# Performance work log

Measured on AMD Instinct MI355X. Metric: run time of the kernel, lower is better.

Reference implementation:

```python
import jax, jax.numpy as jnp
import numpy as np

EPS = 1e-5
NEG_SLOPE = 0.2

def _linear(x, w, b):
    return x @ w.T + b

def _seg_softmax(a, dst, n):
    # numerically stable softmax over edges grouped by destination node
    m = jax.ops.segment_max(a, dst, num_segments=n)
    e = jnp.exp(a - m[dst])
    s = jax.ops.segment_sum(e, dst, num_segments=n)
    return e / (s[dst] + 1e-16)

def _gat(x, src, dst, n, w, a_src, a_dst, b):
    # PyG GATConv, heads=1: h = xW^T; alpha = LeakyReLU(a_s.h_src + a_d.h_dst)
    h = x @ w.T                                   # [N,H]
    al_s = (h * a_src).sum(-1)                    # [N]
    al_d = (h * a_dst).sum(-1)                    # [N]
    alpha = jax.nn.leaky_relu(al_s[src] + al_d[dst], NEG_SLOPE)  # [E]
    attn = _seg_softmax(alpha, dst, n)
    out = jax.ops.segment_sum(attn[:, None] * h[src], dst, num_segments=n)
    return out + b

def _bn(x, g, b):
    # BatchNorm over the node dimension (training-style batch stats, eval dropout)
    mu = x.mean(0)
    var = x.var(0)
    return (x - mu) * jax.lax.rsqrt(var + EPS) * g + b

def setup_inputs() -> dict:
    key = jax.random.key(0)
    N, E, SAT, NEI, H, OUT = 50000, 1600000, 32, 32, 128, 16
    ks = jax.random.split(key, 26)
    p = lambda k, shape, s=0.05: jax.random.normal(k, shape, jnp.float32) * s
    return {
        "x": jax.random.normal(ks[0], (N, SAT + NEI), jnp.float32),
        "edge_index": jax.random.randint(ks[1], (2, E), 0, N, jnp.int32),
        "sat_w": p(ks[2], (H, SAT)), "sat_b": jnp.zeros((H,), jnp.float32),
        "neigh_w": p(ks[3], (H, NEI)), "neigh_b": jnp.zeros((H,), jnp.float32),
        "fus_w": p(ks[4], (1, 2 * H)), "fus_b": jnp.zeros((1,), jnp.float32),
        "w1": p(ks[5], (H, H)), "as1": p(ks[6], (H,)), "ad1": p(ks[7], (H,)), "b1": jnp.zeros((H,), jnp.float32),
        "g1": jnp.ones((H,), jnp.float32), "be1": jnp.zeros((H,), jnp.float32),
        "w2": p(ks[8], (H, H)), "as2": p(ks[9], (H,)), "ad2": p(ks[10], (H,)), "b2": jnp.zeros((H,), jnp.float32),
        "g2": jnp.ones((H,), jnp.float32), "be2": jnp.zeros((H,), jnp.float32),
        "fc1_w": p(ks[11], (H, H)), "fc1_b": jnp.zeros((H,), jnp.float32),
        "fc2_w": p(ks[12], (OUT, H)), "fc2_b": jnp.zeros((OUT,), jnp.float32),
    }

def reference(x, edge_index, sat_w, sat_b, neigh_w, neigh_b, fus_w, fus_b,
              w1, as1, ad1, b1, g1, be1, w2, as2, ad2, b2, g2, be2,
              fc1_w, fc1_b, fc2_w, fc2_b):
    n = x.shape[0]
    sat_dim = sat_w.shape[1]
    sat = jax.nn.relu(_linear(x[:, :sat_dim], sat_w, sat_b))
    nei = jax.nn.relu(_linear(x[:, sat_dim:], neigh_w, neigh_b))
    gate = jax.nn.sigmoid(_linear(jnp.concatenate([sat, nei], axis=1), fus_w, fus_b))
    h = gate * sat + (1.0 - gate) * nei
    # GATConv adds self-loops by default
    loops = jnp.arange(n, dtype=edge_index.dtype)
    src = jnp.concatenate([edge_index[0], loops])
    dst = jnp.concatenate([edge_index[1], loops])
    res = h
    h = jax.nn.relu(_bn(_gat(h, src, dst, n, w1, as1, ad1, b1), g1, be1)) + res
    res = h
    h = jax.nn.relu(_bn(_gat(h, src, dst, n, w2, as2, ad2, b2), g2, be2)) + res
    h = jax.nn.relu(_linear(h, fc1_w, fc1_b))
    return _linear(h, fc2_w, fc2_b)
```

## Files before the change

kernel.cpp:

```cpp
#include <hip/hip_runtime.h>

#define H 128

typedef __attribute__((ext_vector_type(8))) short bf16x8;
typedef __attribute__((ext_vector_type(4))) float f32x4;

__device__ __forceinline__ float bf2f(unsigned short u) {
    return __uint_as_float(((unsigned)u) << 16);
}
__device__ __forceinline__ unsigned short f2bf(float f) {
    unsigned u = __float_as_uint(f);
    unsigned r = (u + 0x7fffu + ((u >> 16) & 1u)) >> 16;
    return (unsigned short)r;
}
__device__ __forceinline__ unsigned pack2bf(float a, float b) {
    return (unsigned)f2bf(a) | ((unsigned)f2bf(b) << 16);
}

__global__ void fill_u32(unsigned* __restrict__ p, unsigned v, int n) {
    int i = blockIdx.x * blockDim.x + threadIdx.x;
    if (i < n) p[i] = v;
}

__global__ void fuse_kernel(const float* __restrict__ x,
                            const float* __restrict__ sat_w, const float* __restrict__ sat_b,
                            const float* __restrict__ neigh_w, const float* __restrict__ neigh_b,
                            const float* __restrict__ fus_w, const float* __restrict__ fus_b,
                            unsigned short* __restrict__ h0b, int N) {
    __shared__ unsigned smem[8512];
    __shared__ float reds[4][64];
    unsigned* a_lds = smem;
    unsigned* w_lds = smem + 2304;
    int tid = threadIdx.x;
    int base = blockIdx.x * 64;
    for (int i = tid; i < 64 * 32; i += 256) {
        int n = i >> 5, kp = i & 31;
        int gn = base + n;
        float2 v = (gn < N) ? *(const float2*)(x + (size_t)gn * 64 + kp * 2) : make_float2(0.f, 0.f);
        a_lds[n * 36 + kp] = pack2bf(v.x, v.y);
    }
    for (int i = tid; i < 256 * 16; i += 256) {
        int r = i >> 4, kp = i & 15;
        const float* wsrc = (r < 128) ? (sat_w + (size_t)r * 32) : (neigh_w + (size_t)(r - 128) * 32);
        float2 v = *(const float2*)(wsrc + kp * 2);
        w_lds[r * 20 + kp] = pack2bf(v.x, v.y);
    }
    __syncthreads();
    int lane = tid & 63;
    int wv = tid >> 6;
    int lr = lane & 15, lk = lane >> 4;
    f32x4 accS[4][2], accN[4][2];
#pragma unroll
    for (int r = 0; r < 4; ++r)
#pragma unroll
        for (int t = 0; t < 2; ++t) {
            accS[r][t] = (f32x4){0.f, 0.f, 0.f, 0.f};
            accN[r][t] = (f32x4){0.f, 0.f, 0.f, 0.f};
        }
    bf16x8 afS[4], afN[4];
#pragma unroll
    for (int r = 0; r < 4; ++r) {
        afS[r] = *(const bf16x8*)&a_lds[(r * 16 + lr) * 36 + lk * 4];
        afN[r] = *(const bf16x8*)&a_lds[(r * 16 + lr) * 36 + 16 + lk * 4];
    }
#pragma unroll
    for (int t = 0; t < 2; ++t) {
        bf16x8 bS = *(const bf16x8*)&w_lds[(wv * 32 + t * 16 + lr) * 20 + lk * 4];
        bf16x8 bN = *(const bf16x8*)&w_lds[(128 + wv * 32 + t * 16 + lr) * 20 + lk * 4];
#pragma unroll
        for (int r = 0; r < 4; ++r) {
            accS[r][t] = __builtin_amdgcn_mfma_f32_16x16x32_bf16(afS[r], bS, accS[r][t], 0, 0, 0);
            accN[r][t] = __builtin_amdgcn_mfma_f32_16x16x32_bf16(afN[r], bN, accN[r][t], 0, 0, 0);
        }
    }
    __syncthreads();
    unsigned short* cst = (unsigned short*)smem;
#pragma unroll
    for (int t = 0; t < 2; ++t) {
        int col = wv * 32 + t * 16 + lr;
        float sb = sat_b[col], nb = neigh_b[col];
#pragma unroll
        for (int r = 0; r < 4; ++r) {
#pragma unroll
            for (int j = 0; j < 4; ++j) {
                int srow = r * 16 + lk * 4 + j;
                cst[srow * 266 + col] = f2bf(fmaxf(accS[r][t][j] + sb, 0.f));
                cst[srow * 266 + 133 + col] = f2bf(fmaxf(accN[r][t][j] + nb, 0.f));
            }
        }
    }
    __syncthreads();
    int node = tid & 63;
    int part = tid >> 6;
    float ps = 0.f;
#pragma unroll
    for (int k = 0; k < 32; ++k) {
        int col = part * 32 + k;
        ps += bf2f(cst[node * 266 + col]) * fus_w[col]
            + bf2f(cst[node * 266 + 133 + col]) * fus_w[128 + col];
    }
    reds[part][node] = ps;
    __syncthreads();
    float tot = reds[0][node] + reds[1][node] + reds[2][node] + reds[3][node];
    float g = 1.f / (1.f + __expf(-(tot + fus_b[0])));
    if (base + node < N) {
        unsigned* op = (unsigned*)h0b + (size_t)(base + node) * 64 + part * 16;
#pragma unroll
        for (int kp = 0; kp < 16; ++kp) {
            int col = part * 32 + kp * 2;
            float o0 = g * bf2f(cst[node * 266 + col]) + (1.f - g) * bf2f(cst[node * 266 + 133 + col]);
            float o1 = g * bf2f(cst[node * 266 + col + 1]) + (1.f - g) * bf2f(cst[node * 266 + 134 + col]);
            op[kp] = pack2bf(o0, o1);
        }
    }
}

template <int TAG, int MODE>
__global__ void gemm128m(const void* __restrict__ inv, const float* __restrict__ w,
                         const float* __restrict__ bias, int do_relu,
                         unsigned short* __restrict__ outb, int N,
                         const float* __restrict__ a_sp, const float* __restrict__ a_dp,
                         float* __restrict__ al_s, float* __restrict__ al_d,
                         const float* __restrict__ bns, const unsigned short* __restrict__ resb,
                         unsigned* __restrict__ yout) {
    __shared__ unsigned a_lds[64 * 68];
    __shared__ unsigned w_lds[128 * 68];
    __shared__ float reds[4][64];
    __shared__ float redd[4][64];
    int tid = threadIdx.x;
    int base = blockIdx.x * 64;
    for (int i = tid; i < 64 * 64; i += 256) {
        int n = i >> 6, kp = i & 63;
        int gn = base + n;
        unsigned p = 0u;
        if (gn < N) {
            if (MODE == 1) {
                p = ((const unsigned*)inv)[(size_t)gn * 64 + kp];
            } else {
                float2 v = *(const float2*)((const float*)inv + (size_t)gn * 128 + kp * 2);
                float2 sc = ((const float2*)bns)[kp];
                float2 sh = ((const float2*)(bns + 128))[kp];
                ushort2 rr = ((const ushort2*)(resb + (size_t)gn * 128))[kp];
                float y0 = fmaxf(v.x * sc.x + sh.x, 0.f) + bf2f(rr.x);
                float y1 = fmaxf(v.y * sc.y + sh.y, 0.f) + bf2f(rr.y);
                p = pack2bf(y0, y1);
                if (yout) yout[(size_t)gn * 64 + kp] = p;
            }
        }
        a_lds[n * 68 + kp] = p;
    }
    for (int i = tid; i < 128 * 64; i += 256) {
        int c = i >> 6, kp = i & 63;
        float2 v = *(const float2*)(w + (size_t)c * 128 + kp * 2);
        w_lds[c * 68 + kp] = pack2bf(v.x, v.y);
    }
    __syncthreads();
    int lane = tid & 63;
    int wv = tid >> 6;
    int lr = lane & 15;
    int lk = lane >> 4;
    f32x4 acc[4][2];
#pragma unroll
    for (int r = 0; r < 4; ++r)
#pragma unroll
        for (int t = 0; t < 2; ++t) acc[r][t] = (f32x4){0.f, 0.f, 0.f, 0.f};
    for (int c = 0; c < 4; ++c) {
        bf16x8 af[4], bfr[2];
#pragma unroll
        for (int r = 0; r < 4; ++r)
            af[r] = *(const bf16x8*)&a_lds[(r * 16 + lr) * 68 + c * 16 + lk * 4];
#pragma unroll
        for (int t = 0; t < 2; ++t)
            bfr[t] = *(const bf16x8*)&w_lds[(wv * 32 + t * 16 + lr) * 68 + c * 16 + lk * 4];
#pragma unroll
        for (int r = 0; r < 4; ++r)
#pragma unroll
            for (int t = 0; t < 2; ++t)
                acc[r][t] = __builtin_amdgcn_mfma_f32_16x16x32_bf16(af[r], bfr[t], acc[r][t], 0, 0, 0);
    }
    __syncthreads();
    unsigned short* cst = (unsigned short*)a_lds;
#pragma unroll
    for (int t = 0; t < 2; ++t) {
        int col = wv * 32 + t * 16 + lr;
        float bv = bias ? bias[col] : 0.f;
#pragma unroll
        for (int r = 0; r < 4; ++r) {
#pragma unroll
            for (int j = 0; j < 4; ++j) {
                float v = acc[r][t][j] + bv;
                if (do_relu) v = fmaxf(v, 0.f);
                cst[(r * 16 + lk * 4 + j) * 136 + col] = f2bf(v);
            }
        }
    }
    __syncthreads();
    for (int i = tid; i < 64 * 64; i += 256) {
        int n = i >> 6, kp = i & 63;
        int gn = base + n;
        if (gn < N) ((unsigned*)outb)[(size_t)gn * 64 + kp] = a_lds[n * 68 + kp];
    }
    if (a_sp) {
        int node = tid & 63;
        int part = tid >> 6;
        float ps = 0.f, pd = 0.f;
        int kb = part * 32;
        const unsigned short* xr = cst + node * 136 + kb;
#pragma unroll
        for (int k = 0; k < 32; ++k) {
            float v = bf2f(xr[k]);
            ps += v * a_sp[kb + k];
            pd += v * a_dp[kb + k];
        }
        reds[part][node] = ps;
        redd[part][node] = pd;
        __syncthreads();
        if (tid < 64) {
            int gn = base + tid;
            if (gn < N) {
                al_s[gn] = reds[0][tid] + reds[1][tid] + reds[2][tid] + reds[3][tid];
                al_d[gn] = redd[0][tid] + redd[1][tid] + redd[2][tid] + redd[3][tid];
            }
        }
    }
}

#define SCB 256
#define NBUK 196
#define BCAP 10240
__global__ void pack_hist_bucket(const int* __restrict__ src, const int* __restrict__ dst,
                                 unsigned* __restrict__ pkb, int* __restrict__ cnt8,
                                 int* __restrict__ bukCur, int E, int N, int CH) {
    __shared__ int lcnt[NBUK];
    __shared__ int lbase[NBUK];
    int tid = threadIdx.x;
    int blk = blockIdx.x;
    int e0 = blk * CH;
    int e1 = min(e0 + CH, E);
    int hcopy = blk & 7;
    for (int sb = e0; sb < e1; sb += 4096) {
        int nsc = min(4096, e1 - sb);
        unsigned pkv[16];
        int rk[16], bb[16];
        for (int i = tid; i < NBUK; i += 256) lcnt[i] = 0;
        __syncthreads();
#pragma unroll
        for (int i = 0; i < 16; ++i) {
            int off = tid + i * 256;
            bb[i] = -1;
            if (off < nsc) {
                int e = sb + off;
                int s = src[e];
                int d = dst[e];
                atomicAdd(cnt8 + (size_t)hcopy * N + d, 1);
                pkv[i] = ((unsigned)d << 16) | (unsigned)s;
                int b = d >> 8;
                bb[i] = b;
                rk[i] = atomicAdd(&lcnt[b], 1);
            }
        }
        __syncthreads();
        for (int i = tid; i < NBUK; i += 256) lbase[i] = atomicAdd(&bukCur[i], lcnt[i]);
        __syncthreads();
#pragma unroll
        for (int i = 0; i < 16; ++i) {
            if (bb[i] >= 0) {
                pkb[(size_t)bb[i] * BCAP + lbase[bb[i]] + rk[i]] = pkv[i];
            }
        }
        __syncthreads();
    }
}

__global__ void scan_a(const int* __restrict__ cnt8, int* __restrict__ nodeoff,
                       int* __restrict__ blocksum, int N) {
    int i = blockIdx.x * SCB + threadIdx.x;
    int tot = 0;
    if (i < N) {
#pragma unroll
        for (int c = 0; c < 8; ++c) tot += cnt8[(size_t)c * N + i];
    }
    __shared__ int tmp[SCB];
    tmp[threadIdx.x] = tot;
    __syncthreads();
    for (int off = 1; off < SCB; off <<= 1) {
        int t = (threadIdx.x >= off) ? tmp[threadIdx.x - off] : 0;
        __syncthreads();
        tmp[threadIdx.x] += t;
        __syncthreads();
    }
    if (i < N) nodeoff[i] = tmp[threadIdx.x] - tot;
    if (threadIdx.x == SCB - 1) blocksum[blockIdx.x] = tmp[SCB - 1];
}

__global__ void scan_b(const int* __restrict__ blocksum, int* __restrict__ blockoff,
                       int* __restrict__ rowptrN, int NB) {
    __shared__ int tmp[1024];
    int t = threadIdx.x;
    int v = (t < NB) ? blocksum[t] : 0;
    tmp[t] = v;
    __syncthreads();
    for (int off = 1; off < 1024; off <<= 1) {
        int u = (t >= off) ? tmp[t - off] : 0;
        __syncthreads();
        tmp[t] += u;
        __syncthreads();
    }
    if (t < NB) blockoff[t] = tmp[t] - v;
    if (t == 1023) *rowptrN = tmp[1023];
}

__global__ void scan_c(const int* __restrict__ nodeoff, const int* __restrict__ blockoff,
                       int* __restrict__ rowptr, float* __restrict__ accum2, int N) {
    if (blockIdx.x < 16) {
        accum2[blockIdx.x * 256 + threadIdx.x] = 0.f;
    }
    int i = blockIdx.x * SCB + threadIdx.x;
    if (i >= N) return;
    rowptr[i] = blockoff[blockIdx.x] + nodeoff[i];
}

__global__ void scatter_sort(const unsigned* __restrict__ pkb, const int* __restrict__ bukCnt,
                             const int* __restrict__ rowptr, int* __restrict__ ssrc, int N) {
    __shared__ int lcur[256];
    __shared__ int tmp[256];
    __shared__ int osrc[BCAP];
    int b = blockIdx.x;
    int d0 = b << 8;
    int cnt = bukCnt[b];
    const unsigned* base = pkb + (size_t)b * BCAP;
    int tid = threadIdx.x;
    lcur[tid] = 0;
    __syncthreads();
    for (int i = tid; i < cnt; i += 256)
        atomicAdd(&lcur[(int)(base[i] >> 16) - d0], 1);
    __syncthreads();
    int v = lcur[tid];
    tmp[tid] = v;
    __syncthreads();
    for (int off = 1; off < 256; off <<= 1) {
        int u = (tid >= off) ? tmp[tid - off] : 0;
        __syncthreads();
        tmp[tid] += u;
        __syncthreads();
    }
    lcur[tid] = tmp[tid] - v;
    __syncthreads();
    for (int i = tid; i < cnt; i += 256) {
        unsigned p = base[i];
        int ld = (int)(p >> 16) - d0;
        int pos = atomicAdd(&lcur[ld], 1);
        osrc[pos] = (int)(p & 0xFFFFu);
    }
    __syncthreads();
    int gbase = rowptr[d0];
    for (int i = tid; i < cnt; i += 256)
        ssrc[gbase + i] = osrc[i];
}

template <int TAG>
__global__ void gat_agg(const int* __restrict__ rowptr, const int* __restrict__ ssrc,
                        const float* __restrict__ al_s, const float* __restrict__ al_d,
                        const unsigned short* __restrict__ hb, float* __restrict__ out,
                        float* __restrict__ accum8, int N) {
    __shared__ int s_sv[4][64];
    __shared__ float s_ev[4][64];
    __shared__ float ys[4][128];
    __shared__ float yq[4][128];
    int tid = threadIdx.x;
    int wiw = tid >> 6;
    int w = (blockIdx.x * blockDim.x + tid) >> 6;
    int lane = tid & 63;
    int sub = lane >> 5;
    int fl = lane & 31;
    float a0 = 0.f, a1 = 0.f, a2 = 0.f, a3 = 0.f;
    float ss = 0.f;
    if (w < N) {
        int beg = rowptr[w], end = rowptr[w + 1];
        float ald = al_d[w];
        float a_self = al_s[w] + ald;
        a_self = (a_self > 0.f) ? a_self : 0.2f * a_self;
        float m = a_self;
        for (int e = beg + lane; e < end; e += 64) {
            float a = al_s[ssrc[e]] + ald;
            a = (a > 0.f) ? a : 0.2f * a;
            m = fmaxf(m, a);
        }
        for (int off = 32; off; off >>= 1) m = fmaxf(m, __shfl_xor(m, off));
        for (int base = beg; base < end; base += 64) {
            int nch = min(64, end - base);
            int sv = 0;
            float ev = 0.f;
            if (lane < nch) {
                sv = ssrc[base + lane];
                float a = al_s[sv] + ald;
                a = (a > 0.f) ? a : 0.2f * a;
                ev = __expf(a - m);
            }
            ss += ev;
            s_sv[wiw][lane] = sv;
            s_ev[wiw][lane] = ev;
            for (int j0 = 0; j0 < nch; j0 += 8) {
                ushort4 hv[4];
                float evv[4];
#pragma unroll
                for (int jj = 0; jj < 4; ++jj) {
                    int j = j0 + 2 * jj + sub;
                    bool ok = j < nch;
                    int svj = ok ? s_sv[wiw][j] : 0;
                    evv[jj] = ok ? s_ev[wiw][j] : 0.f;
                    hv[jj] = ((const ushort4*)(hb + (size_t)svj * H))[fl];
                }
#pragma unroll
                for (int jj = 0; jj < 4; ++jj) {
                    a0 += evv[jj] * bf2f(hv[jj].x);
                    a1 += evv[jj] * bf2f(hv[jj].y);
                    a2 += evv[jj] * bf2f(hv[jj].z);
                    a3 += evv[jj] * bf2f(hv[jj].w);
                }
            }
        }
        for (int off = 32; off; off >>= 1) ss += __shfl_xor(ss, off);
        a0 += __shfl_xor(a0, 32);
        a1 += __shfl_xor(a1, 32);
        a2 += __shfl_xor(a2, 32);
        a3 += __shfl_xor(a3, 32);
        float ev_self = __expf(a_self - m);
        ss += ev_self;
        ushort4 hs = ((const ushort4*)(hb + (size_t)w * H))[fl];
        a0 += ev_self * bf2f(hs.x);
        a1 += ev_self * bf2f(hs.y);
        a2 += ev_self * bf2f(hs.z);
        a3 += ev_self * bf2f(hs.w);
        float inv = 1.f / (ss + 1e-16f);
        a0 *= inv; a1 *= inv; a2 *= inv; a3 *= inv;
        if (sub == 0) {
            ((float4*)(out + (size_t)w * H))[fl] = make_float4(a0, a1, a2, a3);
        }
    }
    if (sub == 0) {
        float4 yy = (w < N) ? make_float4(a0, a1, a2, a3) : make_float4(0.f, 0.f, 0.f, 0.f);
        ((float4*)&ys[wiw][0])[fl] = yy;
        ((float4*)&yq[wiw][0])[fl] = make_float4(yy.x * yy.x, yy.y * yy.y, yy.z * yy.z, yy.w * yy.w);
    }
    __syncthreads();
    if (tid < 128) {
        float s = ys[0][tid] + ys[1][tid] + ys[2][tid] + ys[3][tid];
        float q = yq[0][tid] + yq[1][tid] + yq[2][tid] + yq[3][tid];
        float* ac = accum8 + (size_t)(blockIdx.x & 7) * 256;
        atomicAdd(ac + tid, s);
        atomicAdd(ac + 128 + tid, q);
    }
}

__global__ void bn_finalize(const float* __restrict__ accum8, const float* __restrict__ g,
                            const float* __restrict__ be, float* __restrict__ bns, int N) {
    int tid = threadIdx.x;
    if (tid >= 128) return;
    float s = 0.f, q = 0.f;
#pragma unroll
    for (int c = 0; c < 8; ++c) {
        s += accum8[c * 256 + tid];
        q += accum8[c * 256 + 128 + tid];
    }
    float Ninv = 1.f / (float)N;
    float mu = s * Ninv;
    float var = q * Ninv - mu * mu;
    float rsig = rsqrtf(var + 1e-5f);
    float sc = rsig * g[tid];
    bns[tid] = sc;
    bns[128 + tid] = be[tid] - mu * sc;
}

__global__ void fc2_kernel(const unsigned short* __restrict__ in, const float* __restrict__ w,
                           const float* __restrict__ b, float* __restrict__ out,
                           int N, int OUT) {
    __shared__ float wsm[16 * 132];
    __shared__ float xs[16][129];
    int tid = threadIdx.x;
    for (int i = tid; i < OUT * H; i += 256) {
        int o = i >> 7, k = i & 127;
        wsm[o * 132 + k] = w[i];
    }
    int nb = blockIdx.x * 16;
    for (int i = tid; i < 16 * 128; i += 256) {
        int n = i >> 7, k = i & 127;
        int gn = nb + n;
        xs[n][k] = (gn < N) ? bf2f(in[(size_t)gn * H + k]) : 0.f;
    }
    __syncthreads();
    int o = tid & 15;
    int nn = tid >> 4;
    int n = nb + nn;
    if (n >= N || o >= OUT) return;
    const float* xr = xs[nn];
    const float* wr = wsm + o * 132;
    float acc = b[o];
#pragma unroll 8
    for (int k = 0; k < H; k += 4) {
        acc += xr[k] * wr[k] + xr[k + 1] * wr[k + 1] + xr[k + 2] * wr[k + 2] + xr[k + 3] * wr[k + 3];
    }
    out[(size_t)n * OUT + o] = acc;
}


extern "C" void kernel_launch(void* const* d_in, const int* in_sizes, int n_in,
                              void* d_out, int out_size, void* d_ws, size_t ws_size,
                              hipStream_t stream) {
    const float* x       = (const float*)d_in[0];
    const int*   ei      = (const int*)d_in[1];
    const float* sat_w   = (const float*)d_in[2];
    const float* sat_b   = (const float*)d_in[3];
    const float* neigh_w = (const float*)d_in[4];
    const float* neigh_b = (const float*)d_in[5];
    const float* fus_w   = (const float*)d_in[6];
    const float* fus_b   = (const float*)d_in[7];
    const float* w1      = (const float*)d_in[8];
    const float* as1     = (const float*)d_in[9];
    const float* ad1     = (const float*)d_in[10];
    const float* g1      = (const float*)d_in[12];
    const float* be1     = (const float*)d_in[13];
    const float* w2      = (const float*)d_in[14];
    const float* as2     = (const float*)d_in[15];
    const float* ad2     = (const float*)d_in[16];
    const float* g2      = (const float*)d_in[18];
    const float* be2     = (const float*)d_in[19];
    const float* fc1_w   = (const float*)d_in[20];
    const float* fc1_b   = (const float*)d_in[21];
    const float* fc2_w   = (const float*)d_in[22];
    const float* fc2_b   = (const float*)d_in[23];

    int N = in_sizes[0] / 64;
    int E = in_sizes[1] / 2;
    int OUT = in_sizes[23];
    int NB = (N + SCB - 1) / SCB;
    int CH = (E + 255) / 256;
    int NBUKET = (N + 255) >> 8;

    float* ws    = (float*)d_ws;
    float* h0    = ws;
    float* hA    = h0 + (size_t)N * H;
    float* agg   = hA + (size_t)N * H;
    float* al_s  = agg + (size_t)N * H;
    float* al_d  = al_s + N;
    float* accum = al_d + N;
    float* bns1  = accum + 4096;
    float* bns2  = bns1 + 256;
    int* rowptr  = (int*)(bns2 + 256);
    int* cnt8    = rowptr + (N + 1);
    int* bukCur  = cnt8 + (size_t)8 * N;
    int* nodeoff = bukCur + NBUK;
    int* blocksum= nodeoff + N;
    int* blockoff= blocksum + NB;
    int* ssrc    = blockoff + NB;
    unsigned* pkb= (unsigned*)(ssrc + E);
    unsigned* y1b= pkb + (size_t)NBUK * BCAP;
    unsigned short* hAb = (unsigned short*)hA;
    unsigned short* h0b = (unsigned short*)(hA + (size_t)N * 64);

    const int* srcp = ei;
    const int* dstp = ei + E;

    dim3 b256(256);
    int gGemm = (N + 63) / 64;
    int gWaveN = (N + 3) / 4;

    fuse_kernel<<<gGemm, b256, 0, stream>>>(x, sat_w, sat_b, neigh_w, neigh_b, fus_w, fus_b, h0b, N);

    fill_u32<<<(8 * N + NBUK + 255) / 256, b256, 0, stream>>>((unsigned*)cnt8, 0u, 8 * N + NBUK);
    pack_hist_bucket<<<256, b256, 0, stream>>>(srcp, dstp, pkb, cnt8, bukCur, E, N, CH);
    scan_a<<<NB, SCB, 0, stream>>>(cnt8, nodeoff, blocksum, N);
    scan_b<<<1, 1024, 0, stream>>>(blocksum, blockoff, rowptr + N, NB);
    scan_c<<<NB, SCB, 0, stream>>>(nodeoff, blockoff, rowptr, accum, N);
    scatter_sort<<<NBUKET, b256, 0, stream>>>(pkb, bukCur, rowptr, ssrc, N);

    gemm128m<1, 1><<<gGemm, b256, 0, stream>>>(h0b, w1, nullptr, 0, hAb, N, as1, ad1, al_s, al_d,
                                               nullptr, nullptr, nullptr);
    gat_agg<1><<<gWaveN, b256, 0, stream>>>(rowptr, ssrc, al_s, al_d, hAb, agg, accum, N);
    bn_finalize<<<1, 128, 0, stream>>>(accum, g1, be1, bns1, N);

    gemm128m<2, 2><<<gGemm, b256, 0, stream>>>(agg, w2, nullptr, 0, hAb, N, as2, ad2, al_s, al_d,
                                               bns1, h0b, y1b);
    gat_agg<2><<<gWaveN, b256, 0, stream>>>(rowptr, ssrc, al_s, al_d, hAb, h0, accum + 2048, N);
    bn_finalize<<<1, 128, 0, stream>>>(accum + 2048, g2, be2, bns2, N);

    gemm128m<3, 2><<<gGemm, b256, 0, stream>>>(h0, fc1_w, fc1_b, 1, hAb, N, nullptr, nullptr,
                                               nullptr, nullptr, bns2, (const unsigned short*)y1b,
                                               nullptr);
    fc2_kernel<<<(N + 15) / 16, b256, 0, stream>>>(hAb, fc2_w, fc2_b, (float*)d_out, N, OUT);
}
```

Before: 351.9 us.

## Replace global-atomic CSR build with two-pass local bucket sort

Rebuilds the destination-sorted edge list (CSR) used by the GAT aggregation. Each block now partitions its chunk of edges into 256 buckets in shared memory and records per-block bucket counts and offsets. A single-block kernel then scans the bucket totals, and each bucket block gathers its segments by binary search and computes rowptr locally. This drops the per-node global atomic histogram, the zero-fill and the three-kernel scan, cutting kernel launches and global atomic traffic. In exchange, the bucket-base scan runs serially in one block, and every gathered element pays for a binary search.

```diff
diff --git a/kernel.cpp b/kernel.cpp
--- a/kernel.cpp
+++ b/kernel.cpp
@@ -15,11 +15,6 @@
 }
 __device__ __forceinline__ unsigned pack2bf(float a, float b) {
     return (unsigned)f2bf(a) | ((unsigned)f2bf(b) << 16);
-}
-
-__global__ void fill_u32(unsigned* __restrict__ p, unsigned v, int n) {
-    int i = blockIdx.x * blockDim.x + threadIdx.x;
-    if (i < n) p[i] = v;
 }
 
 __global__ void fuse_kernel(const float* __restrict__ x,
@@ -225,115 +220,107 @@
     }
 }
 
-#define SCB 256
-#define NBUK 196
+#define PBMAX 6400
+#define NBSTR 256
+__global__ void pack_bucket(const int* __restrict__ src, const int* __restrict__ dst,
+                            unsigned* __restrict__ pk2, int* __restrict__ cntBB,
+                            int* __restrict__ offBB, int E, int PB) {
+    __shared__ unsigned opk[PBMAX];
+    __shared__ unsigned opk2[PBMAX];
+    __shared__ int lcnt[256];
+    __shared__ int tmp[256];
+    int tid = threadIdx.x;
+    int blk = blockIdx.x;
+    int e0 = blk * PB;
+    int n = min(PB, E - e0);
+    if (n < 0) n = 0;
+    lcnt[tid] = 0;
+    __syncthreads();
+    for (int i = tid; i < n; i += 256) {
+        int s = src[e0 + i];
+        int d = dst[e0 + i];
+        unsigned p = ((unsigned)d << 16) | (unsigned)s;
+        opk[i] = p;
+        atomicAdd(&lcnt[d >> 8], 1);
+    }
+    __syncthreads();
+    int v = lcnt[tid];
+    tmp[tid] = v;
+    __syncthreads();
+    for (int off = 1; off < 256; off <<= 1) {
+        int u = (tid >= off) ? tmp[tid - off] : 0;
+        __syncthreads();
+        tmp[tid] += u;
+        __syncthreads();
+    }
+    int excl = tmp[tid] - v;
+    cntBB[(size_t)blk * NBSTR + tid] = v;
+    offBB[(size_t)blk * NBSTR + tid] = excl;
+    lcnt[tid] = excl;
+    __syncthreads();
+    for (int i = tid; i < n; i += 256) {
+        unsigned p = opk[i];
+        int pos = atomicAdd(&lcnt[(p >> 16) >> 8], 1);
+        opk2[pos] = p;
+    }
+    __syncthreads();
+    for (int i = tid; i < n; i += 256) pk2[e0 + i] = opk2[i];
+}
+
+__global__ void bucket_base(const int* __restrict__ cntBB, int* __restrict__ bbase,
+                            int* __restrict__ rowptr, float* __restrict__ accum,
+                            int E, int N, int NBLK) {
+    __shared__ int tmp[256];
+    int tid = threadIdx.x;
+    for (int i = tid; i < 4096; i += 256) accum[i] = 0.f;
+    int tot = 0;
+    for (int blk = 0; blk < NBLK; ++blk) tot += cntBB[(size_t)blk * NBSTR + tid];
+    tmp[tid] = tot;
+    __syncthreads();
+    for (int off = 1; off < 256; off <<= 1) {
+        int u = (tid >= off) ? tmp[tid - off] : 0;
+        __syncthreads();
+        tmp[tid] += u;
+        __syncthreads();
+    }
+    bbase[tid] = tmp[tid] - tot;
+    if (tid == 0) rowptr[N] = E;
+}
+
 #define BCAP 10240
-__global__ void pack_hist_bucket(const int* __restrict__ src, const int* __restrict__ dst,
-                                 unsigned* __restrict__ pkb, int* __restrict__ cnt8,
-                                 int* __restrict__ bukCur, int E, int N, int CH) {
-    __shared__ int lcnt[NBUK];
-    __shared__ int lbase[NBUK];
-    int tid = threadIdx.x;
-    int blk = blockIdx.x;
-    int e0 = blk * CH;
-    int e1 = min(e0 + CH, E);
-    int hcopy = blk & 7;
-    for (int sb = e0; sb < e1; sb += 4096) {
-        int nsc = min(4096, e1 - sb);
-        unsigned pkv[16];
-        int rk[16], bb[16];
-        for (int i = tid; i < NBUK; i += 256) lcnt[i] = 0;
-        __syncthreads();
-#pragma unroll
-        for (int i = 0; i < 16; ++i) {
-            int off = tid + i * 256;
-            bb[i] = -1;
-            if (off < nsc) {
-                int e = sb + off;
-                int s = src[e];
-                int d = dst[e];
-                atomicAdd(cnt8 + (size_t)hcopy * N + d, 1);
-                pkv[i] = ((unsigned)d << 16) | (unsigned)s;
-                int b = d >> 8;
-                bb[i] = b;
-                rk[i] = atomicAdd(&lcnt[b], 1);
-            }
-        }
-        __syncthreads();
-        for (int i = tid; i < NBUK; i += 256) lbase[i] = atomicAdd(&bukCur[i], lcnt[i]);
-        __syncthreads();
-#pragma unroll
-        for (int i = 0; i < 16; ++i) {
-            if (bb[i] >= 0) {
-                pkb[(size_t)bb[i] * BCAP + lbase[bb[i]] + rk[i]] = pkv[i];
-            }
-        }
-        __syncthreads();
-    }
-}
-
-__global__ void scan_a(const int* __restrict__ cnt8, int* __restrict__ nodeoff,
-                       int* __restrict__ blocksum, int N) {
-    int i = blockIdx.x * SCB + threadIdx.x;
-    int tot = 0;
-    if (i < N) {
-#pragma unroll
-        for (int c = 0; c < 8; ++c) tot += cnt8[(size_t)c * N + i];
-    }
-    __shared__ int tmp[SCB];
-    tmp[threadIdx.x] = tot;
-    __syncthreads();
-    for (int off = 1; off < SCB; off <<= 1) {
-        int t = (threadIdx.x >= off) ? tmp[threadIdx.x - off] : 0;
-        __syncthreads();
-        tmp[threadIdx.x] += t;
-        __syncthreads();
-    }
-    if (i < N) nodeoff[i] = tmp[threadIdx.x] - tot;
-    if (threadIdx.x == SCB - 1) blocksum[blockIdx.x] = tmp[SCB - 1];
-}
-
-__global__ void scan_b(const int* __restrict__ blocksum, int* __restrict__ blockoff,
-                       int* __restrict__ rowptrN, int NB) {
-    __shared__ int tmp[1024];
-    int t = threadIdx.x;
-    int v = (t < NB) ? blocksum[t] : 0;
-    tmp[t] = v;
-    __syncthreads();
-    for (int off = 1; off < 1024; off <<= 1) {
-        int u = (t >= off) ? tmp[t - off] : 0;
-        __syncthreads();
-        tmp[t] += u;
-        __syncthreads();
-    }
-    if (t < NB) blockoff[t] = tmp[t] - v;
-    if (t == 1023) *rowptrN = tmp[1023];
-}
-
-__global__ void scan_c(const int* __restrict__ nodeoff, const int* __restrict__ blockoff,
-                       int* __restrict__ rowptr, float* __restrict__ accum2, int N) {
-    if (blockIdx.x < 16) {
-        accum2[blockIdx.x * 256 + threadIdx.x] = 0.f;
-    }
-    int i = blockIdx.x * SCB + threadIdx.x;
-    if (i >= N) return;
-    rowptr[i] = blockoff[blockIdx.x] + nodeoff[i];
-}
-
-__global__ void scatter_sort(const unsigned* __restrict__ pkb, const int* __restrict__ bukCnt,
-                             const int* __restrict__ rowptr, int* __restrict__ ssrc, int N) {
+__global__ void scatter_sort2(const unsigned* __restrict__ pk2, const int* __restrict__ cntBB,
+                              const int* __restrict__ offBB, const int* __restrict__ bbase,
+                              int* __restrict__ ssrc, int* __restrict__ rowptr,
+                              int N, int PB) {
+    __shared__ int segoff[257];
+    __shared__ int segsrc[256];
     __shared__ int lcur[256];
     __shared__ int tmp[256];
     __shared__ int osrc[BCAP];
     int b = blockIdx.x;
     int d0 = b << 8;
-    int cnt = bukCnt[b];
-    const unsigned* base = pkb + (size_t)b * BCAP;
-    int tid = threadIdx.x;
+    int tid = threadIdx.x;
+    int c = cntBB[(size_t)tid * NBSTR + b];
+    segsrc[tid] = tid * PB + offBB[(size_t)tid * NBSTR + b];
+    tmp[tid] = c;
     lcur[tid] = 0;
     __syncthreads();
-    for (int i = tid; i < cnt; i += 256)
-        atomicAdd(&lcur[(int)(base[i] >> 16) - d0], 1);
+    for (int off = 1; off < 256; off <<= 1) {
+        int u = (tid >= off) ? tmp[tid - off] : 0;
+        __syncthreads();
+        tmp[tid] += u;
+        __syncthreads();
+    }
+    segoff[tid] = tmp[tid] - c;
+    if (tid == 255) segoff[256] = tmp[255];
+    __syncthreads();
+    int cntb = segoff[256];
+    for (int i = tid; i < cntb; i += 256) {
+        int lo = 0, hi = 255;
+        while (lo < hi) { int mid = (lo + hi + 1) >> 1; if (segoff[mid] <= i) lo = mid; else hi = mid - 1; }
+        unsigned p = pk2[segsrc[lo] + (i - segoff[lo])];
+        atomicAdd(&lcur[(int)(p >> 16) - d0], 1);
+    }
     __syncthreads();
     int v = lcur[tid];
     tmp[tid] = v;
@@ -344,18 +331,20 @@
         tmp[tid] += u;
         __syncthreads();
     }
-    lcur[tid] = tmp[tid] - v;
-    __syncthreads();
-    for (int i = tid; i < cnt; i += 256) {
-        unsigned p = base[i];
-        int ld = (int)(p >> 16) - d0;
-        int pos = atomicAdd(&lcur[ld], 1);
+    int excl = tmp[tid] - v;
+    int gbase = bbase[b];
+    if (d0 + tid < N) rowptr[d0 + tid] = gbase + excl;
+    lcur[tid] = excl;
+    __syncthreads();
+    for (int i = tid; i < cntb; i += 256) {
+        int lo = 0, hi = 255;
+        while (lo < hi) { int mid = (lo + hi + 1) >> 1; if (segoff[mid] <= i) lo = mid; else hi = mid - 1; }
+        unsigned p = pk2[segsrc[lo] + (i - segoff[lo])];
+        int pos = atomicAdd(&lcur[(int)(p >> 16) - d0], 1);
         osrc[pos] = (int)(p & 0xFFFFu);
     }
     __syncthreads();
-    int gbase = rowptr[d0];
-    for (int i = tid; i < cnt; i += 256)
-        ssrc[gbase + i] = osrc[i];
+    for (int i = tid; i < cntb; i += 256) ssrc[gbase + i] = osrc[i];
 }
 
 template <int TAG>
@@ -533,8 +522,7 @@
     int N = in_sizes[0] / 64;
     int E = in_sizes[1] / 2;
     int OUT = in_sizes[23];
-    int NB = (N + SCB - 1) / SCB;
-    int CH = (E + 255) / 256;
+    int PB = (E + 255) / 256;
     int NBUKET = (N + 255) >> 8;
 
     float* ws    = (float*)d_ws;
@@ -547,14 +535,12 @@
     float* bns1  = accum + 4096;
     float* bns2  = bns1 + 256;
     int* rowptr  = (int*)(bns2 + 256);
-    int* cnt8    = rowptr + (N + 1);
-    int* bukCur  = cnt8 + (size_t)8 * N;
-    int* nodeoff = bukCur + NBUK;
-    int* blocksum= nodeoff + N;
-    int* blockoff= blocksum + NB;
-    int* ssrc    = blockoff + NB;
-    unsigned* pkb= (unsigned*)(ssrc + E);
-    unsigned* y1b= pkb + (size_t)NBUK * BCAP;
+    int* cntBB   = rowptr + (N + 1);
+    int* offBB   = cntBB + 256 * NBSTR;
+    int* bbase   = offBB + 256 * NBSTR;
+    int* ssrc    = bbase + 256;
+    unsigned* pk2= (unsigned*)(ssrc + E);
+    unsigned* y1b= pk2 + E;
     unsigned short* hAb = (unsigned short*)hA;
     unsigned short* h0b = (unsigned short*)(hA + (size_t)N * 64);
 
@@ -567,12 +553,9 @@
 
     fuse_kernel<<<gGemm, b256, 0, stream>>>(x, sat_w, sat_b, neigh_w, neigh_b, fus_w, fus_b, h0b, N);
 
-    fill_u32<<<(8 * N + NBUK + 255) / 256, b256, 0, stream>>>((unsigned*)cnt8, 0u, 8 * N + NBUK);
-    pack_hist_bucket<<<256, b256, 0, stream>>>(srcp, dstp, pkb, cnt8, bukCur, E, N, CH);
-    scan_a<<<NB, SCB, 0, stream>>>(cnt8, nodeoff, blocksum, N);
-    scan_b<<<1, 1024, 0, stream>>>(blocksum, blockoff, rowptr + N, NB);
-    scan_c<<<NB, SCB, 0, stream>>>(nodeoff, blockoff, rowptr, accum, N);
-    scatter_sort<<<NBUKET, b256, 0, stream>>>(pkb, bukCur, rowptr, ssrc, N);
+    pack_bucket<<<256, b256, 0, stream>>>(srcp, dstp, pk2, cntBB, offBB, E, PB);
+    bucket_base<<<1, b256, 0, stream>>>(cntBB, bbase, rowptr, accum, E, N, 256);
+    scatter_sort2<<<NBUKET, b256, 0, stream>>>(pk2, cntBB, offBB, bbase, ssrc, rowptr, N, PB);
 
     gemm128m<1, 1><<<gGemm, b256, 0, stream>>>(h0b, w1, nullptr, 0, hAb, N, as1, ad1, al_s, al_d,
                                                nullptr, nullptr, nullptr);
```

After: 352.7 us. About the same (+0.2%).
